# Kernel optimization log

Hardware: AMD Instinct MI355X
Metric: run time of the kernel (lower is better)

The kernel has to match this reference:

```python
import jax, jax.numpy as jnp
import numpy as np

N, E, IN_F, H1, F1, H2, F2, OUT_F = 50000, 800000, 128, 4, 32, 1, 64, 2
NEG_SLOPE = 0.2  # PyG GATConv default


def setup_inputs() -> dict:
    key = jax.random.key(0)
    ks = jax.random.split(key, 10)
    p = lambda k, shp: jax.random.normal(k, shp, jnp.float32) * 0.1
    return {
        "x": jax.random.normal(ks[0], (N, IN_F), jnp.float32),
        "edge_index": jax.random.randint(ks[1], (2, E), 0, N),
        "W1": p(ks[2], (IN_F, H1 * F1)),
        "att_s1": p(ks[3], (H1, F1)),
        "att_d1": p(ks[4], (H1, F1)),
        "b1": jnp.zeros((H1 * F1,), jnp.float32),
        "W2": p(ks[5], (H1 * F1, H2 * F2)),
        "att_s2": p(ks[6], (H2, F2)),
        "att_d2": p(ks[7], (H2, F2)),
        "b2": jnp.zeros((F2,), jnp.float32),
        "Wl": p(ks[8], (F2, OUT_F)),
        "bl": jnp.zeros((OUT_F,), jnp.float32),
    }


def _gat_conv(x, src, dst, W, att_s, att_d, bias, concat):
    # PyG GATConv: per-head linear, leaky-relu attention logits,
    # segment-softmax over incoming edges of each dst, scatter-add aggregate.
    n = x.shape[0]
    H, F = att_s.shape
    h = (x @ W).reshape(n, H, F)                        # [N, H, F]
    a_s = jnp.einsum('nhf,hf->nh', h, att_s)            # [N, H]
    a_d = jnp.einsum('nhf,hf->nh', h, att_d)
    logits = jax.nn.leaky_relu(a_s[src] + a_d[dst], NEG_SLOPE)  # [Etot, H]
    m = jax.ops.segment_max(logits, dst, num_segments=n)
    e = jnp.exp(logits - m[dst])
    denom = jax.ops.segment_sum(e, dst, num_segments=n)
    alpha = e / denom[dst]                              # segment softmax
    msg = h[src] * alpha[:, :, None]                    # [Etot, H, F]
    out = jax.ops.segment_sum(msg, dst, num_segments=n)  # [N, H, F]
    out = out.reshape(n, H * F) if concat else out.mean(axis=1)
    return out + bias


def reference(x, edge_index, W1, att_s1, att_d1, b1, W2, att_s2, att_d2, b2, Wl, bl):
    n = x.shape[0]
    loops = jnp.arange(n, dtype=edge_index.dtype)       # add_self_loops=True
    src = jnp.concatenate([edge_index[0], loops])
    dst = jnp.concatenate([edge_index[1], loops])
    h = jax.nn.elu(_gat_conv(x, src, dst, W1, att_s1, att_d1, b1, True))
    h = jax.nn.elu(_gat_conv(h, src, dst, W2, att_s2, att_d2, b2, False))
    pooled = h.sum(axis=0, keepdims=True)               # global_add_pool, batch=0
    out = pooled @ Wl + bl
    return pooled, out
```

## Files before the change

### kernel.cpp

```cpp
#include <hip/hip_runtime.h>

#define N_NODES 50000
#define N_EDGES 800000
#define NB 196
#define P1_BLOCKS 256
#define EPB 3125
#define BH_SIZE (NB * P1_BLOCKS)
#define GEMM_BLOCKS ((N_NODES + 63) / 64)

__device__ __forceinline__ float lrelu(float x) { return fmaxf(x, 0.2f * x); }
__device__ __forceinline__ float elu(float x) { return x > 0.f ? x : __expf(x) - 1.f; }

typedef float f32x2 __attribute__((ext_vector_type(2)));

__device__ __forceinline__ float bfl(unsigned u) { return __uint_as_float(u << 16); }
__device__ __forceinline__ float bfh(unsigned u) { return __uint_as_float(u & 0xffff0000u); }
__device__ __forceinline__ unsigned f2bf_rn(float x) {
  unsigned u = __float_as_uint(x);
  return (u + 0x7fffu + ((u >> 16) & 1u)) >> 16;
}
__device__ __forceinline__ unsigned pack2bf(float a, float b) {
  return f2bf_rn(a) | (f2bf_rn(b) << 16);
}

__device__ __forceinline__ int block_excl_scan(int v, int* total_out) {
  int lane = threadIdx.x & 63;
  int wid = threadIdx.x >> 6;
  int x = v;
#pragma unroll
  for (int off = 1; off < 64; off <<= 1) {
    int u = __shfl_up(x, off);
    if (lane >= off) x += u;
  }
  __shared__ int wsum[4];
  if (lane == 63) wsum[wid] = x;
  __syncthreads();
  int add = 0;
#pragma unroll
  for (int k = 0; k < 4; ++k)
    if (k < wid) add += wsum[k];
  if (total_out) *total_out = wsum[0] + wsum[1] + wsum[2] + wsum[3];
  return x + add - v;
}

__global__ __launch_bounds__(256) void hist1_kernel(const int* __restrict__ ei, int* __restrict__ bh) {
  __shared__ int cnt[NB];
  for (int t = threadIdx.x; t < NB; t += 256) cnt[t] = 0;
  __syncthreads();
  int start = blockIdx.x * EPB;
  for (int i = start + threadIdx.x; i < start + EPB; i += 256)
    atomicAdd(&cnt[ei[N_EDGES + i] >> 8], 1);
  __syncthreads();
  for (int t = threadIdx.x; t < NB; t += 256)
    bh[t * P1_BLOCKS + blockIdx.x] = cnt[t];
}

__global__ __launch_bounds__(256) void scan_part_kernel(const int* __restrict__ bh, int* __restrict__ bhP,
                                                        int* __restrict__ blocksum) {
  int g = blockIdx.x * 256 + threadIdx.x;
  int v = bh[g];
  int total;
  int ex = block_excl_scan(v, &total);
  bhP[g] = ex;
  if (threadIdx.x == 0) blocksum[blockIdx.x] = total;
}

__global__ __launch_bounds__(256) void scan_top_kernel(const int* __restrict__ blocksum, int* __restrict__ blockoff) {
  int t = threadIdx.x;
  int v = (t < NB) ? blocksum[t] : 0;
  int ex = block_excl_scan(v, nullptr);
  if (t < NB) blockoff[t] = ex;
}

__global__ __launch_bounds__(256) void scatter1_kernel(const int* __restrict__ ei, const int* __restrict__ bhP,
                                                       const int* __restrict__ blockoff, int2* __restrict__ eb) {
  __shared__ int cur[NB];
  for (int t = threadIdx.x; t < NB; t += 256) cur[t] = 0;
  __syncthreads();
  int start = blockIdx.x * EPB;
  for (int i = start + threadIdx.x; i < start + EPB; i += 256) {
    int dst = ei[N_EDGES + i];
    int src = ei[i];
    int bin = dst >> 8;
    int r = atomicAdd(&cur[bin], 1);
    int idx = bin * P1_BLOCKS + blockIdx.x;
    int pos = bhP[idx] + blockoff[bin] + r;
    eb[pos] = make_int2(src, dst);
  }
}

__global__ __launch_bounds__(256) void bucket_csr_kernel(const int2* __restrict__ eb, const int* __restrict__ blockoff,
                                                         int* __restrict__ rowptrF, int* __restrict__ col) {
  __shared__ int cnt[256];
  __shared__ int basel[256];
  __shared__ int cur[256];
  int b = blockIdx.x;
  int t = threadIdx.x;
  cnt[t] = 0;
  cur[t] = 0;
  __syncthreads();
  int start = blockoff[b];
  int end = (b == NB - 1) ? N_EDGES : blockoff[b + 1];
  for (int i = start + t; i < end; i += 256)
    atomicAdd(&cnt[eb[i].y & 255], 1);
  __syncthreads();
  int ex = block_excl_scan(cnt[t], nullptr);
  basel[t] = start + ex;
  int g = b * 256 + t;
  if (g < N_NODES) rowptrF[g] = start + ex;
  if (g == N_NODES) rowptrF[N_NODES] = N_EDGES;
  __syncthreads();
  for (int i = start + t; i < end; i += 256) {
    int2 e = eb[i];
    int d8 = e.y & 255;
    int r = atomicAdd(&cur[d8], 1);
    col[basel[d8] + r] = e.x;
  }
}

#define XS_STRIDE 36
template <int COLS, bool ABF16>
__device__ __forceinline__ void gemm_body(int bx, const void* __restrict__ Ap, const float* __restrict__ W,
                                          const float* __restrict__ atts, const float* __restrict__ attd,
                                          unsigned* __restrict__ Yb, float* __restrict__ as_out,
                                          float* __restrict__ ad_out) {
  constexpr int CPT = COLS / 16;
  constexpr int G = COLS / 4;
  __shared__ float ws[32 * COLS];
  __shared__ float xs[64 * XS_STRIDE];
  int t = threadIdx.x;
  int rbase = bx * 64;
  int tx = t & 15, ty = t >> 4;
  float acc[4][CPT];
#pragma unroll
  for (int r = 0; r < 4; ++r)
#pragma unroll
    for (int c = 0; c < CPT; ++c) acc[r][c] = 0.f;

  const float4* W4 = (const float4*)W;
  float4* ws4 = (float4*)ws;
  for (int kt = 0; kt < 4; ++kt) {
    for (int i = t; i < 32 * G; i += 256) {
      int k = i / G;
      int g = i - k * G;
      int c4g = g & (CPT / 4 - 1);
      int txg = g / (CPT / 4);
      ws4[k * G + c4g * 16 + txg] = W4[kt * 32 * G + i];
    }
    if constexpr (ABF16) {
      const uint4* A4 = (const uint4*)Ap;
      {
        int i = t;
        int row = i >> 2, q = i & 3;
        int gr = rbase + row; if (gr >= N_NODES) gr = N_NODES - 1;
        uint4 u = A4[gr * 16 + kt * 4 + q];
        float4 lo = make_float4(bfl(u.x), bfh(u.x), bfl(u.y), bfh(u.y));
        float4 hi = make_float4(bfl(u.z), bfh(u.z), bfl(u.w), bfh(u.w));
        float4* dst = (float4*)&xs[row * XS_STRIDE + q * 8];
        dst[0] = lo; dst[1] = hi;
      }
    } else {
      const float4* A4 = (const float4*)Ap;
      for (int i = t; i < 512; i += 256) {
        int row = i >> 3, kc = i & 7;
        int gr = rbase + row; if (gr >= N_NODES) gr = N_NODES - 1;
        *(float4*)&xs[row * XS_STRIDE + kc * 4] = A4[gr * 32 + kt * 8 + kc];
      }
    }
    __syncthreads();
#pragma unroll 8
    for (int k = 0; k < 32; ++k) {
      float xr[4];
#pragma unroll
      for (int r = 0; r < 4; ++r) xr[r] = xs[(ty * 4 + r) * XS_STRIDE + k];
#pragma unroll
      for (int c4 = 0; c4 < CPT / 4; ++c4) {
        float4 wv = ws4[k * G + c4 * 16 + tx];
#pragma unroll
        for (int r = 0; r < 4; ++r) {
          acc[r][c4 * 4 + 0] += xr[r] * wv.x;
          acc[r][c4 * 4 + 1] += xr[r] * wv.y;
          acc[r][c4 * 4 + 2] += xr[r] * wv.z;
          acc[r][c4 * 4 + 3] += xr[r] * wv.w;
        }
      }
    }
    __syncthreads();
  }

  if constexpr (COLS == 128) {
    int h = tx >> 2;
    int base = h * 32 + (tx & 3) * 8;
#pragma unroll
    for (int r = 0; r < 4; ++r) {
      float ps = 0.f, pd = 0.f;
#pragma unroll
      for (int c = 0; c < 8; ++c) {
        ps += acc[r][c] * atts[base + c];
        pd += acc[r][c] * attd[base + c];
      }
      ps += __shfl_xor(ps, 1); pd += __shfl_xor(pd, 1);
      ps += __shfl_xor(ps, 2); pd += __shfl_xor(pd, 2);
      int row = rbase + ty * 4 + r;
      if ((tx & 3) == 0 && row < N_NODES) {
        as_out[row * 4 + h] = ps;
        ad_out[row * 4 + h] = pd;
      }
    }
  } else {
#pragma unroll
    for (int r = 0; r < 4; ++r) {
      float ps = 0.f, pd = 0.f;
#pragma unroll
      for (int c = 0; c < 4; ++c) {
        ps += acc[r][c] * atts[tx * 4 + c];
        pd += acc[r][c] * attd[tx * 4 + c];
      }
#pragma unroll
      for (int off = 1; off < 16; off <<= 1) {
        ps += __shfl_xor(ps, off);
        pd += __shfl_xor(pd, off);
      }
      int row = rbase + ty * 4 + r;
      if (tx == 0 && row < N_NODES) {
        as_out[row] = ps;
        ad_out[row] = pd;
      }
    }
  }

#pragma unroll
  for (int r = 0; r < 4; ++r) {
    int row = rbase + ty * 4 + r;
    if (row < N_NODES) {
      if constexpr (CPT == 8) {
        unsigned lo = __builtin_amdgcn_cvt_pk_fp8_f32(acc[r][0], acc[r][1], 0, false);
        lo = __builtin_amdgcn_cvt_pk_fp8_f32(acc[r][2], acc[r][3], lo, true);
        unsigned hi = __builtin_amdgcn_cvt_pk_fp8_f32(acc[r][4], acc[r][5], 0, false);
        hi = __builtin_amdgcn_cvt_pk_fp8_f32(acc[r][6], acc[r][7], hi, true);
        ((uint2*)Yb)[row * 16 + tx] = make_uint2(lo, hi);
      } else {
        unsigned u = __builtin_amdgcn_cvt_pk_fp8_f32(acc[r][0], acc[r][1], 0, false);
        u = __builtin_amdgcn_cvt_pk_fp8_f32(acc[r][2], acc[r][3], u, true);
        Yb[row * 16 + tx] = u;
      }
    }
  }
}

__global__ __launch_bounds__(256) void gemm128_kernel(const float* __restrict__ x, const float* __restrict__ W1,
                                                      const float* __restrict__ atts, const float* __restrict__ attd,
                                                      unsigned* __restrict__ h1b, float* __restrict__ as1,
                                                      float* __restrict__ ad1) {
  gemm_body<128, false>(blockIdx.x, x, W1, atts, attd, h1b, as1, ad1);
}

__global__ __launch_bounds__(256) void gemm64_kernel(const unsigned* __restrict__ h1eb, const float* __restrict__ W2,
                                                     const float* __restrict__ atts, const float* __restrict__ attd,
                                                     unsigned* __restrict__ h2b, float* __restrict__ as2,
                                                     float* __restrict__ ad2) {
  gemm_body<64, true>(blockIdx.x, h1eb, W2, atts, attd, h2b, as2, ad2);
}

__global__ __launch_bounds__(256) void agg1_kernel(const uint2* __restrict__ h1f8, const int* __restrict__ rowptr,
                                                   const int* __restrict__ col, const float* __restrict__ as1,
                                                   const float* __restrict__ ad1, const float4* __restrict__ b1v,
                                                   uint4* __restrict__ h1eb4) {
  int n = (blockIdx.x * 256 + threadIdx.x) >> 6;
  int lane = threadIdx.x & 63;
  int slot = lane >> 4;
  int fo = lane & 15;
  int h = fo >> 2;
  int beg = rowptr[n], end = rowptr[n + 1];
  float adh = ad1[n * 4 + h];

  f32x2 acc2[4];
#pragma unroll
  for (int j = 0; j < 4; ++j) acc2[j] = (f32x2){0.f, 0.f};
  float esum = 0.f;

#define ACC_EDGE1(E)                                               \
  {                                                                \
    int src = col[E];                                              \
    float a = __expf(lrelu(as1[src * 4 + h] + adh));               \
    esum += a;                                                     \
    f32x2 av = {a, a};                                             \
    uint2 uu = h1f8[src * 16 + fo];                                \
    f32x2 p0 = __builtin_amdgcn_cvt_pk_f32_fp8(uu.x, false);       \
    f32x2 p1 = __builtin_amdgcn_cvt_pk_f32_fp8(uu.x, true);        \
    f32x2 p2 = __builtin_amdgcn_cvt_pk_f32_fp8(uu.y, false);       \
    f32x2 p3 = __builtin_amdgcn_cvt_pk_f32_fp8(uu.y, true);        \
    acc2[0] += av * p0; acc2[1] += av * p1;                        \
    acc2[2] += av * p2; acc2[3] += av * p3;                        \
  }

  int i = beg;
  for (; i + 16 <= end; i += 16) {
#pragma unroll
    for (int u = 0; u < 4; ++u) ACC_EDGE1(i + u * 4 + slot);
  }
  for (; i + 4 <= end; i += 4) ACC_EDGE1(i + slot);
  int rem = end - i;
  if (slot < rem) ACC_EDGE1(i + slot);
#undef ACC_EDGE1
  if (slot == 0) {
    float a = __expf(lrelu(as1[n * 4 + h] + adh));
    esum += a;
    f32x2 av = {a, a};
    uint2 uu = h1f8[n * 16 + fo];
    f32x2 p0 = __builtin_amdgcn_cvt_pk_f32_fp8(uu.x, false);
    f32x2 p1 = __builtin_amdgcn_cvt_pk_f32_fp8(uu.x, true);
    f32x2 p2 = __builtin_amdgcn_cvt_pk_f32_fp8(uu.y, false);
    f32x2 p3 = __builtin_amdgcn_cvt_pk_f32_fp8(uu.y, true);
    acc2[0] += av * p0; acc2[1] += av * p1;
    acc2[2] += av * p2; acc2[3] += av * p3;
  }
#pragma unroll
  for (int j = 0; j < 4; ++j) {
    acc2[j].x += __shfl_xor(acc2[j].x, 16);
    acc2[j].y += __shfl_xor(acc2[j].y, 16);
    acc2[j].x += __shfl_xor(acc2[j].x, 32);
    acc2[j].y += __shfl_xor(acc2[j].y, 32);
  }
  esum += __shfl_xor(esum, 16);
  esum += __shfl_xor(esum, 32);
  if (slot == 0) {
    float dsc = 1.f / esum;
    float4 b0 = b1v[fo * 2], b1 = b1v[fo * 2 + 1];
    float f0 = elu(acc2[0].x * dsc + b0.x), f1 = elu(acc2[0].y * dsc + b0.y);
    float f2 = elu(acc2[1].x * dsc + b0.z), f3 = elu(acc2[1].y * dsc + b0.w);
    float f4 = elu(acc2[2].x * dsc + b1.x), f5 = elu(acc2[2].y * dsc + b1.y);
    float f6 = elu(acc2[3].x * dsc + b1.z), f7 = elu(acc2[3].y * dsc + b1.w);
    uint4 o;
    o.x = pack2bf(f0, f1); o.y = pack2bf(f2, f3);
    o.z = pack2bf(f4, f5); o.w = pack2bf(f6, f7);
    h1eb4[n * 16 + fo] = o;
  }
}

__global__ __launch_bounds__(256) void agg2_kernel(const uint2* __restrict__ h2f8, const int* __restrict__ rowptr,
                                                   const int* __restrict__ col, const float* __restrict__ as2,
                                                   const float* __restrict__ ad2, const float4* __restrict__ b2v,
                                                   float* __restrict__ pooled) {
  __shared__ float red[4][64];
  int n = (blockIdx.x * 256 + threadIdx.x) >> 6;
  int lane = threadIdx.x & 63;
  int wid = threadIdx.x >> 6;
  int slot = lane >> 3;
  int fo = lane & 7;
  int beg = rowptr[n], end = rowptr[n + 1];
  float ad = ad2[n];

  f32x2 acc2[4];
#pragma unroll
  for (int j = 0; j < 4; ++j) acc2[j] = (f32x2){0.f, 0.f};
  float esum = 0.f;

#define ACC_EDGE2(E)                                               \
  {                                                                \
    int src = col[E];                                              \
    float a = __expf(lrelu(as2[src] + ad));                        \
    esum += a;                                                     \
    f32x2 av = {a, a};                                             \
    uint2 uu = h2f8[src * 8 + fo];                                 \
    f32x2 p0 = __builtin_amdgcn_cvt_pk_f32_fp8(uu.x, false);       \
    f32x2 p1 = __builtin_amdgcn_cvt_pk_f32_fp8(uu.x, true);        \
    f32x2 p2 = __builtin_amdgcn_cvt_pk_f32_fp8(uu.y, false);       \
    f32x2 p3 = __builtin_amdgcn_cvt_pk_f32_fp8(uu.y, true);        \
    acc2[0] += av * p0; acc2[1] += av * p1;                        \
    acc2[2] += av * p2; acc2[3] += av * p3;                        \
  }

  int i = beg;
  for (; i + 32 <= end; i += 32) {
#pragma unroll
    for (int u = 0; u < 4; ++u) ACC_EDGE2(i + u * 8 + slot);
  }
  for (; i + 8 <= end; i += 8) ACC_EDGE2(i + slot);
  int rem = end - i;
  if (slot < rem) ACC_EDGE2(i + slot);
#undef ACC_EDGE2
  if (slot == 0) {
    float a = __expf(lrelu(as2[n] + ad));
    esum += a;
    f32x2 av = {a, a};
    uint2 uu = h2f8[n * 8 + fo];
    f32x2 p0 = __builtin_amdgcn_cvt_pk_f32_fp8(uu.x, false);
    f32x2 p1 = __builtin_amdgcn_cvt_pk_f32_fp8(uu.x, true);
    f32x2 p2 = __builtin_amdgcn_cvt_pk_f32_fp8(uu.y, false);
    f32x2 p3 = __builtin_amdgcn_cvt_pk_f32_fp8(uu.y, true);
    acc2[0] += av * p0; acc2[1] += av * p1;
    acc2[2] += av * p2; acc2[3] += av * p3;
  }
#pragma unroll
  for (int j = 0; j < 4; ++j) {
#pragma unroll
    for (int off = 8; off <= 32; off <<= 1) {
      acc2[j].x += __shfl_xor(acc2[j].x, off);
      acc2[j].y += __shfl_xor(acc2[j].y, off);
    }
  }
  esum += __shfl_xor(esum, 8);
  esum += __shfl_xor(esum, 16);
  esum += __shfl_xor(esum, 32);
  if (slot == 0) {
    float dsc = 1.f / esum;
    float4 b0 = b2v[fo * 2], b1 = b2v[fo * 2 + 1];
    red[wid][fo * 8 + 0] = elu(acc2[0].x * dsc + b0.x);
    red[wid][fo * 8 + 1] = elu(acc2[0].y * dsc + b0.y);
    red[wid][fo * 8 + 2] = elu(acc2[1].x * dsc + b0.z);
    red[wid][fo * 8 + 3] = elu(acc2[1].y * dsc + b0.w);
    red[wid][fo * 8 + 4] = elu(acc2[2].x * dsc + b1.x);
    red[wid][fo * 8 + 5] = elu(acc2[2].y * dsc + b1.y);
    red[wid][fo * 8 + 6] = elu(acc2[3].x * dsc + b1.z);
    red[wid][fo * 8 + 7] = elu(acc2[3].y * dsc + b1.w);
  }
  __syncthreads();
  if (threadIdx.x < 64) {
    float sum = red[0][threadIdx.x] + red[1][threadIdx.x] + red[2][threadIdx.x] + red[3][threadIdx.x];
    atomicAdd(&pooled[(blockIdx.x & 63) * 64 + threadIdx.x], sum);
  }
}

__global__ void final_kernel(const float* __restrict__ pooledS, const float* __restrict__ Wl,
                             const float* __restrict__ bl, float* __restrict__ out) {
  __shared__ float p[64];
  int t = threadIdx.x;
  float v = 0.f;
  for (int k = 0; k < 64; ++k) v += pooledS[k * 64 + t];
  p[t] = v;
  out[t] = v;
  __syncthreads();
  if (t < 2) {
    float s = bl[t];
    for (int k = 0; k < 64; ++k) s += p[k] * Wl[k * 2 + t];
    out[64 + t] = s;
  }
}

extern "C" void kernel_launch(void* const* d_in, const int* in_sizes, int n_in,
                              void* d_out, int out_size, void* d_ws, size_t ws_size,
                              hipStream_t stream) {
  (void)in_sizes; (void)n_in; (void)out_size; (void)ws_size;
  const float* x     = (const float*)d_in[0];
  const int*   ei    = (const int*)d_in[1];
  const float* W1    = (const float*)d_in[2];
  const float* atts1 = (const float*)d_in[3];
  const float* attd1 = (const float*)d_in[4];
  const float* b1    = (const float*)d_in[5];
  const float* W2    = (const float*)d_in[6];
  const float* atts2 = (const float*)d_in[7];
  const float* attd2 = (const float*)d_in[8];
  const float* b2    = (const float*)d_in[9];
  const float* Wl    = (const float*)d_in[10];
  const float* bl    = (const float*)d_in[11];
  float* out = (float*)d_out;

  char* w = (char*)d_ws;
  unsigned* h1b  = (unsigned*)w; w += (size_t)N_NODES * 128;
  unsigned* h1eb = (unsigned*)w; w += (size_t)N_NODES * 128 * 2;
  unsigned* h2b  = (unsigned*)w; w += (size_t)N_NODES * 64;
  float* as1  = (float*)w; w += (size_t)N_NODES * 16;
  float* ad1  = (float*)w; w += (size_t)N_NODES * 16;
  float* as2  = (float*)w; w += (size_t)N_NODES * 4;
  float* ad2  = (float*)w; w += (size_t)N_NODES * 4;
  float* pooled = (float*)w; w += 64 * 64 * 4;
  int* rowptrF = (int*)w; w += (size_t)(N_NODES + 1) * 4 + 12;
  int* col    = (int*)w; w += (size_t)N_EDGES * 4;
  int2* eb    = (int2*)w; w += (size_t)N_EDGES * 8;
  int* bh     = (int*)w; w += (size_t)BH_SIZE * 4;
  int* bhP    = (int*)w; w += (size_t)BH_SIZE * 4;
  int* blocksum = (int*)w; w += 256 * 4;
  int* blockoff = (int*)w; w += 256 * 4;

  (void)hipMemsetAsync(pooled, 0, 64 * 64 * 4, stream);

  hist1_kernel<<<P1_BLOCKS, 256, 0, stream>>>(ei, bh);
  scan_part_kernel<<<BH_SIZE / 256, 256, 0, stream>>>(bh, bhP, blocksum);
  scan_top_kernel<<<1, 256, 0, stream>>>(blocksum, blockoff);
  scatter1_kernel<<<P1_BLOCKS, 256, 0, stream>>>(ei, bhP, blockoff, eb);
  bucket_csr_kernel<<<NB, 256, 0, stream>>>(eb, blockoff, rowptrF, col);

  gemm128_kernel<<<GEMM_BLOCKS, 256, 0, stream>>>(x, W1, atts1, attd1, h1b, as1, ad1);
  agg1_kernel<<<N_NODES / 4, 256, 0, stream>>>((const uint2*)h1b, rowptrF, col, as1, ad1,
                                               (const float4*)b1, (uint4*)h1eb);

  gemm64_kernel<<<GEMM_BLOCKS, 256, 0, stream>>>(h1eb, W2, atts2, attd2, h2b, as2, ad2);
  agg2_kernel<<<N_NODES / 4, 256, 0, stream>>>((const uint2*)h2b, rowptrF, col, as2, ad2,
                                               (const float4*)b2, pooled);

  final_kernel<<<1, 64, 0, stream>>>(pooled, Wl, bl, out);
}
```

Measured before the change: 231.4 us.

## Use bf16 MFMA GEMMs with folded attention columns and fuse launch chain

Both dense projections now run on bf16 MFMA 16x16x32 instructions instead of scalar FP32 FMAs. Weights are pre-packed in a setup kernel that also folds the attention vectors into extra weight columns, so the attention logits come out of the same matmul. The launch chain is shortened: the histogram is fused with weight packing, the partial scan with the first GEMM, and the top-level scan is recomputed inside scatter and bucket kernels. The final pooling is done by the last aggregation block through an atomic counter. This trades extra bf16 rounding of inputs and weights, and of the folded attention logits, for fewer launches and cheaper matmuls.

Measured after the change: 432.3 us. 1.87x slower.

```diff
diff --git a/kernel.cpp b/kernel.cpp
--- a/kernel.cpp
+++ b/kernel.cpp
@@ -7,20 +7,27 @@
 #define EPB 3125
 #define BH_SIZE (NB * P1_BLOCKS)
 #define GEMM_BLOCKS ((N_NODES + 63) / 64)
+#define AGG_BLOCKS (N_NODES / 4)
 
 __device__ __forceinline__ float lrelu(float x) { return fmaxf(x, 0.2f * x); }
 __device__ __forceinline__ float elu(float x) { return x > 0.f ? x : __expf(x) - 1.f; }
 
 typedef float f32x2 __attribute__((ext_vector_type(2)));
-
-__device__ __forceinline__ float bfl(unsigned u) { return __uint_as_float(u << 16); }
-__device__ __forceinline__ float bfh(unsigned u) { return __uint_as_float(u & 0xffff0000u); }
+typedef float f32x4v __attribute__((ext_vector_type(4)));
+typedef short bf16x8 __attribute__((ext_vector_type(8)));
+
 __device__ __forceinline__ unsigned f2bf_rn(float x) {
   unsigned u = __float_as_uint(x);
   return (u + 0x7fffu + ((u >> 16) & 1u)) >> 16;
 }
 __device__ __forceinline__ unsigned pack2bf(float a, float b) {
   return f2bf_rn(a) | (f2bf_rn(b) << 16);
+}
+__device__ __forceinline__ uint4 pack8bf(const float* v) {
+  uint4 o;
+  o.x = pack2bf(v[0], v[1]); o.y = pack2bf(v[2], v[3]);
+  o.z = pack2bf(v[4], v[5]); o.w = pack2bf(v[6], v[7]);
+  return o;
 }
 
 __device__ __forceinline__ int block_excl_scan(int v, int* total_out) {
@@ -43,64 +50,226 @@
   return x + add - v;
 }
 
-__global__ __launch_bounds__(256) void hist1_kernel(const int* __restrict__ ei, int* __restrict__ bh) {
+__global__ __launch_bounds__(256) void setup_hist_kernel(
+    const int* __restrict__ ei, int* __restrict__ bh,
+    const float* __restrict__ W1, const float* __restrict__ atts1, const float* __restrict__ attd1,
+    const float* __restrict__ W2, const float* __restrict__ atts2, const float* __restrict__ attd2,
+    uint4* __restrict__ Wpk1, uint4* __restrict__ Wpk2) {
   __shared__ int cnt[NB];
-  for (int t = threadIdx.x; t < NB; t += 256) cnt[t] = 0;
+  int bid = blockIdx.x;
+  if (bid >= 2) {
+    for (int t = threadIdx.x; t < NB; t += 256) cnt[t] = 0;
+    __syncthreads();
+    int start = (bid - 2) * EPB;
+    for (int i = start + threadIdx.x; i < start + EPB; i += 256)
+      atomicAdd(&cnt[ei[N_EDGES + i] >> 8], 1);
+    __syncthreads();
+    for (int t = threadIdx.x; t < NB; t += 256)
+      bh[t * P1_BLOCKS + (bid - 2)] = cnt[t];
+    return;
+  }
+  if (bid == 0) {
+    for (int s = threadIdx.x; s < 4 * 9 * 64; s += 256) {
+      int l = s & 63, sf = s >> 6;
+      int f = sf % 9, ks = sf / 9;
+      int colb = f * 16 + (l & 15);
+      int kb = ks * 32 + ((l >> 4) << 3);
+      float v[8];
+      if (colb < 128) {
+#pragma unroll
+        for (int j = 0; j < 8; ++j) v[j] = W1[(kb + j) * 128 + colb];
+      } else if (colb < 136) {
+        int cc = colb - 128;
+        const float* at = (cc < 4) ? atts1 : attd1;
+        int h = cc & 3;
+#pragma unroll
+        for (int j = 0; j < 8; ++j) {
+          float s2 = 0.f;
+          for (int q = 0; q < 32; ++q) s2 += W1[(kb + j) * 128 + h * 32 + q] * at[h * 32 + q];
+          v[j] = s2;
+        }
+      } else {
+#pragma unroll
+        for (int j = 0; j < 8; ++j) v[j] = 0.f;
+      }
+      Wpk1[s] = pack8bf(v);
+    }
+  } else {
+    for (int s = threadIdx.x; s < 4 * 5 * 64; s += 256) {
+      int l = s & 63, sf = s >> 6;
+      int f = sf % 5, ks = sf / 5;
+      int colb = f * 16 + (l & 15);
+      int kb = ks * 32 + ((l >> 4) << 3);
+      float v[8];
+      if (colb < 64) {
+#pragma unroll
+        for (int j = 0; j < 8; ++j) v[j] = W2[(kb + j) * 64 + colb];
+      } else if (colb < 66) {
+        const float* at = (colb == 64) ? atts2 : attd2;
+#pragma unroll
+        for (int j = 0; j < 8; ++j) {
+          float s2 = 0.f;
+          for (int q = 0; q < 64; ++q) s2 += W2[(kb + j) * 64 + q] * at[q];
+          v[j] = s2;
+        }
+      } else {
+#pragma unroll
+        for (int j = 0; j < 8; ++j) v[j] = 0.f;
+      }
+      Wpk2[s] = pack8bf(v);
+    }
+  }
+}
+
+template <int NF, bool ABF16>
+__device__ __forceinline__ void mfma_gemm_body(int bx, const void* __restrict__ Ap,
+                                               const uint4* __restrict__ Wpk,
+                                               unsigned* __restrict__ Yb,
+                                               float* __restrict__ as_out, float* __restrict__ ad_out) {
+  __shared__ unsigned short Xs[64 * 136];
+  __shared__ uint4 Ws[NF * 256];
+  int t = threadIdx.x;
+  int rbase = bx * 64;
+#pragma unroll
+  for (int p = 0; p < NF; ++p) Ws[p * 256 + t] = Wpk[p * 256 + t];
+  if constexpr (ABF16) {
+    const uint4* A4 = (const uint4*)Ap;
+#pragma unroll
+    for (int p = 0; p < 4; ++p) {
+      int i = p * 256 + t;
+      int row = i >> 4, q = i & 15;
+      int gr = rbase + row; if (gr > N_NODES - 1) gr = N_NODES - 1;
+      *(uint4*)&Xs[row * 136 + q * 8] = A4[gr * 16 + q];
+    }
+  } else {
+    const float4* A4 = (const float4*)Ap;
+#pragma unroll
+    for (int p = 0; p < 8; ++p) {
+      int i = p * 256 + t;
+      int row = i >> 5, q = i & 31;
+      int gr = rbase + row; if (gr > N_NODES - 1) gr = N_NODES - 1;
+      float4 v = A4[gr * 32 + q];
+      *(uint2*)&Xs[row * 136 + q * 4] = make_uint2(pack2bf(v.x, v.y), pack2bf(v.z, v.w));
+    }
+  }
+  __syncthreads();
+
+  int l = t & 63, wv = t >> 6;
+  int lc = l & 15, lk = l >> 4;
+  f32x4v acc[NF];
+#pragma unroll
+  for (int f = 0; f < NF; ++f) acc[f] = (f32x4v){0.f, 0.f, 0.f, 0.f};
+  const unsigned short* ap = &Xs[(wv * 16 + lc) * 136 + lk * 8];
+#pragma unroll
+  for (int ks = 0; ks < 4; ++ks) {
+    bf16x8 a = *(const bf16x8*)(ap + ks * 32);
+#pragma unroll
+    for (int f = 0; f < NF; ++f) {
+      bf16x8 b = *(const bf16x8*)&Ws[(ks * NF + f) * 64 + l];
+      acc[f] = __builtin_amdgcn_mfma_f32_16x16x32_bf16(a, b, acc[f], 0, 0, 0);
+    }
+  }
+
+  constexpr int NCF = NF - 1;
+#pragma unroll
+  for (int reg = 0; reg < 4; ++reg) {
+    int row = rbase + wv * 16 + lk * 4 + reg;
+    bool rok = row < N_NODES;
+    float av = acc[NCF][reg];
+    if (rok) {
+      if constexpr (NF == 9) {
+        if (lc < 4) as_out[row * 4 + lc] = av;
+        else if (lc < 8) ad_out[row * 4 + lc - 4] = av;
+      } else {
+        if (lc == 0) as_out[row] = av;
+        else if (lc == 1) ad_out[row] = av;
+      }
+    }
+    unsigned words[NCF];
+#pragma unroll
+    for (int f = 0; f < NCF; ++f) {
+      float v = acc[f][reg];
+      float n1 = __shfl_xor(v, 1);
+      unsigned pk = (unsigned)__builtin_amdgcn_cvt_pk_fp8_f32(v, n1, 0, false);
+      unsigned pk2 = (unsigned)__shfl_xor((int)pk, 2);
+      words[f] = (pk & 0xffffu) | (pk2 << 16);
+    }
+    if (rok && (lc & 3) == 0) {
+#pragma unroll
+      for (int f = 0; f < NCF; ++f)
+        Yb[row * (NCF * 4) + f * 4 + (lc >> 2)] = words[f];
+    }
+  }
+}
+
+__global__ __launch_bounds__(256) void gemm128_scan_kernel(
+    const float* __restrict__ x, const uint4* __restrict__ Wpk1,
+    unsigned* __restrict__ h1b, float* __restrict__ as1, float* __restrict__ ad1,
+    const int* __restrict__ bh, int* __restrict__ bhP, int* __restrict__ blocksum) {
+  if (blockIdx.x < GEMM_BLOCKS) {
+    mfma_gemm_body<9, false>(blockIdx.x, x, Wpk1, h1b, as1, ad1);
+  } else {
+    int b = blockIdx.x - GEMM_BLOCKS;
+    int g = b * 256 + threadIdx.x;
+    int v = bh[g];
+    int total;
+    int ex = block_excl_scan(v, &total);
+    bhP[g] = ex;
+    if (threadIdx.x == 0) blocksum[b] = total;
+  }
+}
+
+__global__ __launch_bounds__(256) void gemm64_kernel(const uint4* __restrict__ h1eb,
+                                                     const uint4* __restrict__ Wpk2,
+                                                     unsigned* __restrict__ h2b,
+                                                     float* __restrict__ as2, float* __restrict__ ad2) {
+  mfma_gemm_body<5, true>(blockIdx.x, h1eb, Wpk2, h2b, as2, ad2);
+}
+
+__global__ __launch_bounds__(256) void scatter1_kernel(const int* __restrict__ ei, const int* __restrict__ bhP,
+                                                       const int* __restrict__ blocksum, int2* __restrict__ eb) {
+  __shared__ int cur[NB];
+  __shared__ int boff[NB];
+  int t = threadIdx.x;
+  for (int i = t; i < NB; i += 256) cur[i] = 0;
+  {
+    int v = (t < NB) ? blocksum[t] : 0;
+    int ex = block_excl_scan(v, nullptr);
+    if (t < NB) boff[t] = ex;
+  }
   __syncthreads();
   int start = blockIdx.x * EPB;
-  for (int i = start + threadIdx.x; i < start + EPB; i += 256)
-    atomicAdd(&cnt[ei[N_EDGES + i] >> 8], 1);
-  __syncthreads();
-  for (int t = threadIdx.x; t < NB; t += 256)
-    bh[t * P1_BLOCKS + blockIdx.x] = cnt[t];
-}
-
-__global__ __launch_bounds__(256) void scan_part_kernel(const int* __restrict__ bh, int* __restrict__ bhP,
-                                                        int* __restrict__ blocksum) {
-  int g = blockIdx.x * 256 + threadIdx.x;
-  int v = bh[g];
-  int total;
-  int ex = block_excl_scan(v, &total);
-  bhP[g] = ex;
-  if (threadIdx.x == 0) blocksum[blockIdx.x] = total;
-}
-
-__global__ __launch_bounds__(256) void scan_top_kernel(const int* __restrict__ blocksum, int* __restrict__ blockoff) {
-  int t = threadIdx.x;
-  int v = (t < NB) ? blocksum[t] : 0;
-  int ex = block_excl_scan(v, nullptr);
-  if (t < NB) blockoff[t] = ex;
-}
-
-__global__ __launch_bounds__(256) void scatter1_kernel(const int* __restrict__ ei, const int* __restrict__ bhP,
-                                                       const int* __restrict__ blockoff, int2* __restrict__ eb) {
-  __shared__ int cur[NB];
-  for (int t = threadIdx.x; t < NB; t += 256) cur[t] = 0;
-  __syncthreads();
-  int start = blockIdx.x * EPB;
-  for (int i = start + threadIdx.x; i < start + EPB; i += 256) {
+  for (int i = start + t; i < start + EPB; i += 256) {
     int dst = ei[N_EDGES + i];
     int src = ei[i];
     int bin = dst >> 8;
     int r = atomicAdd(&cur[bin], 1);
     int idx = bin * P1_BLOCKS + blockIdx.x;
-    int pos = bhP[idx] + blockoff[bin] + r;
+    int pos = bhP[idx] + boff[bin] + r;
     eb[pos] = make_int2(src, dst);
   }
 }
 
-__global__ __launch_bounds__(256) void bucket_csr_kernel(const int2* __restrict__ eb, const int* __restrict__ blockoff,
+__global__ __launch_bounds__(256) void bucket_csr_kernel(const int2* __restrict__ eb,
+                                                         const int* __restrict__ blocksum,
                                                          int* __restrict__ rowptrF, int* __restrict__ col) {
   __shared__ int cnt[256];
   __shared__ int basel[256];
   __shared__ int cur[256];
+  __shared__ int sse[2];
   int b = blockIdx.x;
   int t = threadIdx.x;
+  {
+    int v = (t < NB) ? blocksum[t] : 0;
+    int ex0 = block_excl_scan(v, nullptr);
+    if (t == b) sse[0] = ex0;
+    if (t == b + 1) sse[1] = ex0;
+  }
   cnt[t] = 0;
   cur[t] = 0;
   __syncthreads();
-  int start = blockoff[b];
-  int end = (b == NB - 1) ? N_EDGES : blockoff[b + 1];
+  int start = sse[0];
+  int end = (b == NB - 1) ? N_EDGES : sse[1];
   for (int i = start + t; i < end; i += 256)
     atomicAdd(&cnt[eb[i].y & 255], 1);
   __syncthreads();
@@ -116,150 +285,6 @@
     int r = atomicAdd(&cur[d8], 1);
     col[basel[d8] + r] = e.x;
   }
-}
-
-#define XS_STRIDE 36
-template <int COLS, bool ABF16>
-__device__ __forceinline__ void gemm_body(int bx, const void* __restrict__ Ap, const float* __restrict__ W,
-                                          const float* __restrict__ atts, const float* __restrict__ attd,
-                                          unsigned* __restrict__ Yb, float* __restrict__ as_out,
-                                          float* __restrict__ ad_out) {
-  constexpr int CPT = COLS / 16;
-  constexpr int G = COLS / 4;
-  __shared__ float ws[32 * COLS];
-  __shared__ float xs[64 * XS_STRIDE];
-  int t = threadIdx.x;
-  int rbase = bx * 64;
-  int tx = t & 15, ty = t >> 4;
-  float acc[4][CPT];
-#pragma unroll
-  for (int r = 0; r < 4; ++r)
-#pragma unroll
-    for (int c = 0; c < CPT; ++c) acc[r][c] = 0.f;
-
-  const float4* W4 = (const float4*)W;
-  float4* ws4 = (float4*)ws;
-  for (int kt = 0; kt < 4; ++kt) {
-    for (int i = t; i < 32 * G; i += 256) {
-      int k = i / G;
-      int g = i - k * G;
-      int c4g = g & (CPT / 4 - 1);
-      int txg = g / (CPT / 4);
-      ws4[k * G + c4g * 16 + txg] = W4[kt * 32 * G + i];
-    }
-    if constexpr (ABF16) {
-      const uint4* A4 = (const uint4*)Ap;
-      {
-        int i = t;
-        int row = i >> 2, q = i & 3;
-        int gr = rbase + row; if (gr >= N_NODES) gr = N_NODES - 1;
-        uint4 u = A4[gr * 16 + kt * 4 + q];
-        float4 lo = make_float4(bfl(u.x), bfh(u.x), bfl(u.y), bfh(u.y));
-        float4 hi = make_float4(bfl(u.z), bfh(u.z), bfl(u.w), bfh(u.w));
-        float4* dst = (float4*)&xs[row * XS_STRIDE + q * 8];
-        dst[0] = lo; dst[1] = hi;
-      }
-    } else {
-      const float4* A4 = (const float4*)Ap;
-      for (int i = t; i < 512; i += 256) {
-        int row = i >> 3, kc = i & 7;
-        int gr = rbase + row; if (gr >= N_NODES) gr = N_NODES - 1;
-        *(float4*)&xs[row * XS_STRIDE + kc * 4] = A4[gr * 32 + kt * 8 + kc];
-      }
-    }
-    __syncthreads();
-#pragma unroll 8
-    for (int k = 0; k < 32; ++k) {
-      float xr[4];
-#pragma unroll
-      for (int r = 0; r < 4; ++r) xr[r] = xs[(ty * 4 + r) * XS_STRIDE + k];
-#pragma unroll
-      for (int c4 = 0; c4 < CPT / 4; ++c4) {
-        float4 wv = ws4[k * G + c4 * 16 + tx];
-#pragma unroll
-        for (int r = 0; r < 4; ++r) {
-          acc[r][c4 * 4 + 0] += xr[r] * wv.x;
-          acc[r][c4 * 4 + 1] += xr[r] * wv.y;
-          acc[r][c4 * 4 + 2] += xr[r] * wv.z;
-          acc[r][c4 * 4 + 3] += xr[r] * wv.w;
-        }
-      }
-    }
-    __syncthreads();
-  }
-
-  if constexpr (COLS == 128) {
-    int h = tx >> 2;
-    int base = h * 32 + (tx & 3) * 8;
-#pragma unroll
-    for (int r = 0; r < 4; ++r) {
-      float ps = 0.f, pd = 0.f;
-#pragma unroll
-      for (int c = 0; c < 8; ++c) {
-        ps += acc[r][c] * atts[base + c];
-        pd += acc[r][c] * attd[base + c];
-      }
-      ps += __shfl_xor(ps, 1); pd += __shfl_xor(pd, 1);
-      ps += __shfl_xor(ps, 2); pd += __shfl_xor(pd, 2);
-      int row = rbase + ty * 4 + r;
-      if ((tx & 3) == 0 && row < N_NODES) {
-        as_out[row * 4 + h] = ps;
-        ad_out[row * 4 + h] = pd;
-      }
-    }
-  } else {
-#pragma unroll
-    for (int r = 0; r < 4; ++r) {
-      float ps = 0.f, pd = 0.f;
-#pragma unroll
-      for (int c = 0; c < 4; ++c) {
-        ps += acc[r][c] * atts[tx * 4 + c];
-        pd += acc[r][c] * attd[tx * 4 + c];
-      }
-#pragma unroll
-      for (int off = 1; off < 16; off <<= 1) {
-        ps += __shfl_xor(ps, off);
-        pd += __shfl_xor(pd, off);
-      }
-      int row = rbase + ty * 4 + r;
-      if (tx == 0 && row < N_NODES) {
-        as_out[row] = ps;
-        ad_out[row] = pd;
-      }
-    }
-  }
-
-#pragma unroll
-  for (int r = 0; r < 4; ++r) {
-    int row = rbase + ty * 4 + r;
-    if (row < N_NODES) {
-      if constexpr (CPT == 8) {
-        unsigned lo = __builtin_amdgcn_cvt_pk_fp8_f32(acc[r][0], acc[r][1], 0, false);
-        lo = __builtin_amdgcn_cvt_pk_fp8_f32(acc[r][2], acc[r][3], lo, true);
-        unsigned hi = __builtin_amdgcn_cvt_pk_fp8_f32(acc[r][4], acc[r][5], 0, false);
-        hi = __builtin_amdgcn_cvt_pk_fp8_f32(acc[r][6], acc[r][7], hi, true);
-        ((uint2*)Yb)[row * 16 + tx] = make_uint2(lo, hi);
-      } else {
-        unsigned u = __builtin_amdgcn_cvt_pk_fp8_f32(acc[r][0], acc[r][1], 0, false);
-        u = __builtin_amdgcn_cvt_pk_fp8_f32(acc[r][2], acc[r][3], u, true);
-        Yb[row * 16 + tx] = u;
-      }
-    }
-  }
-}
-
-__global__ __launch_bounds__(256) void gemm128_kernel(const float* __restrict__ x, const float* __restrict__ W1,
-                                                      const float* __restrict__ atts, const float* __restrict__ attd,
-                                                      unsigned* __restrict__ h1b, float* __restrict__ as1,
-                                                      float* __restrict__ ad1) {
-  gemm_body<128, false>(blockIdx.x, x, W1, atts, attd, h1b, as1, ad1);
-}
-
-__global__ __launch_bounds__(256) void gemm64_kernel(const unsigned* __restrict__ h1eb, const float* __restrict__ W2,
-                                                     const float* __restrict__ atts, const float* __restrict__ attd,
-                                                     unsigned* __restrict__ h2b, float* __restrict__ as2,
-                                                     float* __restrict__ ad2) {
-  gemm_body<64, true>(blockIdx.x, h1eb, W2, atts, attd, h2b, as2, ad2);
 }
 
 __global__ __launch_bounds__(256) void agg1_kernel(const uint2* __restrict__ h1f8, const int* __restrict__ rowptr,
@@ -341,8 +366,12 @@
 __global__ __launch_bounds__(256) void agg2_kernel(const uint2* __restrict__ h2f8, const int* __restrict__ rowptr,
                                                    const int* __restrict__ col, const float* __restrict__ as2,
                                                    const float* __restrict__ ad2, const float4* __restrict__ b2v,
-                                                   float* __restrict__ pooled) {
+                                                   float* __restrict__ pooled, const float* __restrict__ Wl,
+                                                   const float* __restrict__ bl, float* __restrict__ out,
+                                                   int* __restrict__ done) {
   __shared__ float red[4][64];
+  __shared__ float pfin[64];
+  __shared__ int lastf;
   int n = (blockIdx.x * 256 + threadIdx.x) >> 6;
   int lane = threadIdx.x & 63;
   int wid = threadIdx.x >> 6;
@@ -420,21 +449,27 @@
     float sum = red[0][threadIdx.x] + red[1][threadIdx.x] + red[2][threadIdx.x] + red[3][threadIdx.x];
     atomicAdd(&pooled[(blockIdx.x & 63) * 64 + threadIdx.x], sum);
   }
-}
-
-__global__ void final_kernel(const float* __restrict__ pooledS, const float* __restrict__ Wl,
-                             const float* __restrict__ bl, float* __restrict__ out) {
-  __shared__ float p[64];
-  int t = threadIdx.x;
-  float v = 0.f;
-  for (int k = 0; k < 64; ++k) v += pooledS[k * 64 + t];
-  p[t] = v;
-  out[t] = v;
-  __syncthreads();
-  if (t < 2) {
-    float s = bl[t];
-    for (int k = 0; k < 64; ++k) s += p[k] * Wl[k * 2 + t];
-    out[64 + t] = s;
+  __syncthreads();
+  if (threadIdx.x == 0) {
+    __threadfence();
+    lastf = (atomicAdd(done, 1) == AGG_BLOCKS - 1);
+  }
+  __syncthreads();
+  if (lastf) {
+    int t = threadIdx.x;
+    if (t < 64) {
+      float v = 0.f;
+      for (int k = 0; k < 64; ++k)
+        v += __hip_atomic_load(&pooled[k * 64 + t], __ATOMIC_RELAXED, __HIP_MEMORY_SCOPE_AGENT);
+      pfin[t] = v;
+      out[t] = v;
+    }
+    __syncthreads();
+    if (t < 2) {
+      float s = bl[t];
+      for (int k = 0; k < 64; ++k) s += pfin[k] * Wl[k * 2 + t];
+      out[64 + t] = s;
+    }
   }
 }
 
@@ -465,29 +500,25 @@
   float* as2  = (float*)w; w += (size_t)N_NODES * 4;
   float* ad2  = (float*)w; w += (size_t)N_NODES * 4;
   float* pooled = (float*)w; w += 64 * 64 * 4;
+  int* done   = (int*)w; w += 16;
+  uint4* Wpk1 = (uint4*)w; w += 4 * 9 * 64 * 16;
+  uint4* Wpk2 = (uint4*)w; w += 4 * 5 * 64 * 16;
   int* rowptrF = (int*)w; w += (size_t)(N_NODES + 1) * 4 + 12;
   int* col    = (int*)w; w += (size_t)N_EDGES * 4;
   int2* eb    = (int2*)w; w += (size_t)N_EDGES * 8;
   int* bh     = (int*)w; w += (size_t)BH_SIZE * 4;
   int* bhP    = (int*)w; w += (size_t)BH_SIZE * 4;
   int* blocksum = (int*)w; w += 256 * 4;
-  int* blockoff = (int*)w; w += 256 * 4;
-
-  (void)hipMemsetAsync(pooled, 0, 64 * 64 * 4, stream);
-
-  hist1_kernel<<<P1_BLOCKS, 256, 0, stream>>>(ei, bh);
-  scan_part_kernel<<<BH_SIZE / 256, 256, 0, stream>>>(bh, bhP, blocksum);
-  scan_top_kernel<<<1, 256, 0, stream>>>(blocksum, blockoff);
-  scatter1_kernel<<<P1_BLOCKS, 256, 0, stream>>>(ei, bhP, blockoff, eb);
-  bucket_csr_kernel<<<NB, 256, 0, stream>>>(eb, blockoff, rowptrF, col);
-
-  gemm128_kernel<<<GEMM_BLOCKS, 256, 0, stream>>>(x, W1, atts1, attd1, h1b, as1, ad1);
-  agg1_kernel<<<N_NODES / 4, 256, 0, stream>>>((const uint2*)h1b, rowptrF, col, as1, ad1,
-                                               (const float4*)b1, (uint4*)h1eb);
-
-  gemm64_kernel<<<GEMM_BLOCKS, 256, 0, stream>>>(h1eb, W2, atts2, attd2, h2b, as2, ad2);
-  agg2_kernel<<<N_NODES / 4, 256, 0, stream>>>((const uint2*)h2b, rowptrF, col, as2, ad2,
-                                               (const float4*)b2, pooled);
-
-  final_kernel<<<1, 64, 0, stream>>>(pooled, Wl, bl, out);
-}
+
+  (void)hipMemsetAsync(pooled, 0, 64 * 64 * 4 + 16, stream);
+
+  setup_hist_kernel<<<258, 256, 0, stream>>>(ei, bh, W1, atts1, attd1, W2, atts2, attd2, Wpk1, Wpk2);
+  gemm128_scan_kernel<<<GEMM_BLOCKS + NB, 256, 0, stream>>>(x, Wpk1, h1b, as1, ad1, bh, bhP, blocksum);
+  scatter1_kernel<<<P1_BLOCKS, 256, 0, stream>>>(ei, bhP, blocksum, eb);
+  bucket_csr_kernel<<<NB, 256, 0, stream>>>(eb, blocksum, rowptrF, col);
+  agg1_kernel<<<AGG_BLOCKS, 256, 0, stream>>>((const uint2*)h1b, rowptrF, col, as1, ad1,
+                                              (const float4*)b1, (uint4*)h1eb);
+  gemm64_kernel<<<GEMM_BLOCKS, 256, 0, stream>>>((const uint4*)h1eb, Wpk2, h2b, as2, ad2);
+  agg2_kernel<<<AGG_BLOCKS, 256, 0, stream>>>((const uint2*)h2b, rowptrF, col, as2, ad2,
+                                              (const float4*)b2, pooled, Wl, bl, out, done);
+}
```
